# Kernel optimization log

Measured on AMD Instinct MI355X. Metric: run time of the kernel, lower is better.

## Reference

```python
import jax, jax.numpy as jnp
import numpy as np

NUM_EMBEDDINGS = 1024
EMBEDDING_DIM = 256
COMMITMENT_COST = 0.25
DECAY = 0.99
EPS = 1e-5


def setup_inputs() -> dict:
    key = jax.random.key(0)
    k0, k1, k2 = jax.random.split(key, 3)
    x = jax.random.normal(k0, (32, 2048, EMBEDDING_DIM), dtype=jnp.float32)
    # embedding.weight.data.uniform_(-1/K, 1/K)
    embedding_w = jax.random.uniform(
        k1, (NUM_EMBEDDINGS, EMBEDDING_DIM), dtype=jnp.float32,
        minval=-1.0 / NUM_EMBEDDINGS, maxval=1.0 / NUM_EMBEDDINGS)
    ema_cluster_size = jnp.zeros((NUM_EMBEDDINGS,), dtype=jnp.float32)
    ema_w = jax.random.normal(k2, (NUM_EMBEDDINGS, EMBEDDING_DIM), dtype=jnp.float32)
    return {"x": x, "embedding_w": embedding_w,
            "ema_cluster_size": ema_cluster_size, "ema_w": ema_w}


def reference(x, embedding_w, ema_cluster_size, ema_w):
    K, D = embedding_w.shape
    flat = x.reshape(-1, D)  # [N, D]

    # squared L2 distances to codebook: [N, K]
    distances = ((flat * flat).sum(axis=1, keepdims=True)
                 - 2.0 * flat @ embedding_w.T
                 + (embedding_w * embedding_w).sum(axis=1))
    indices = jnp.argmin(distances, axis=1)  # [N] int

    # gather quantized vectors
    quantized = embedding_w[indices].reshape(x.shape)

    # EMA statistics via scatter-add (one-hot.T @ flat without materializing one-hot)
    counts = jax.ops.segment_sum(jnp.ones((flat.shape[0],), dtype=flat.dtype),
                                 indices, num_segments=K)  # [K]
    dw = jax.ops.segment_sum(flat, indices, num_segments=K)  # [K, D]

    new_cluster_size = DECAY * ema_cluster_size + (1.0 - DECAY) * counts
    new_ema_w = DECAY * ema_w + (1.0 - DECAY) * dw

    # Laplace smoothing of cluster sizes, normalized codebook update
    n = new_cluster_size.sum()
    cs = (new_cluster_size + EPS) / (n + K * EPS) * n
    new_embedding_w = new_ema_w / cs[:, None]

    # commitment loss (codebook side is EMA-updated, so only e-latent term)
    e_latent_loss = jnp.mean((jax.lax.stop_gradient(quantized) - x) ** 2)
    loss = COMMITMENT_COST * e_latent_loss

    # straight-through estimator
    quantized_st = x + jax.lax.stop_gradient(quantized - x)

    avg_probs = counts / counts.sum()
    perplexity = jnp.exp(-jnp.sum(avg_probs * jnp.log(avg_probs + 1e-10)))

    return (loss, quantized_st, perplexity,
            new_embedding_w, new_cluster_size, new_ema_w)
```

## Files before the change

### kernel.cpp

```cpp
#include <hip/hip_runtime.h>
#include <math.h>

#define N_ROWS   65536
#define K_EMB    1024
#define D_EMB    256

typedef __attribute__((ext_vector_type(8)))  short short8;
typedef __attribute__((ext_vector_type(4)))  short short4v;
typedef __attribute__((ext_vector_type(16))) float floatx16;

__device__ inline unsigned short f2bf(float f) {
    unsigned u = __float_as_uint(f);
    unsigned r = u + 0x7fffu + ((u >> 16) & 1u);
    return (unsigned short)(r >> 16);
}
__device__ inline float bf2f(unsigned short s) {
    return __uint_as_float(((unsigned)s) << 16);
}

__global__ __launch_bounds__(64)
void prep_e(const float* __restrict__ ew, float* __restrict__ half_esq,
            short* __restrict__ pack_hi, short* __restrict__ pack_lo)
{
    const int k = blockIdx.x;
    const int t = threadIdx.x;
    float4 v = *(const float4*)(ew + (size_t)k * D_EMB + t * 4);
    float s = v.x * v.x + v.y * v.y + v.z * v.z + v.w * v.w;
#pragma unroll
    for (int off = 32; off > 0; off >>= 1) s += __shfl_down(s, off);
    if (t == 0) half_esq[k] = 0.5f * s;

    const int d0   = t * 4;
    const int tile = k >> 5;
    const int kt   = d0 >> 4;
    const int half = (d0 & 15) >> 3;
    const int lane = (k & 31) + 32 * half;
    const int j0   = d0 & 7;
    const int off  = tile * 8192 + kt * 512 + lane * 8 + j0;

    float f[4] = {-v.x, -v.y, -v.z, -v.w};
    short4v h, l;
#pragma unroll
    for (int j = 0; j < 4; ++j) {
        unsigned short hh = f2bf(f[j]);
        h[j] = (short)hh;
        l[j] = (short)f2bf(f[j] - bf2f(hh));
    }
    *(short4v*)(pack_hi + off) = h;
    *(short4v*)(pack_lo + off) = l;
}

__global__ __launch_bounds__(256, 2)
void argmin_mfma(const float* __restrict__ x,
                 const short* __restrict__ pack_hi,
                 const short* __restrict__ pack_lo,
                 const float* __restrict__ half_esq,
                 const float* __restrict__ ew,
                 int* __restrict__ indices,
                 float* __restrict__ out_q,
                 double* __restrict__ loss_buckets)
{
    __shared__ short xs_hi[32 * 256];
    __shared__ short xs_lo[32 * 256];
    __shared__ float cmv[128];
    __shared__ int   cmi[128];
    __shared__ int   widx[32];

    const int t  = threadIdx.x;
    const int r0 = blockIdx.x * 32;

#pragma unroll
    for (int i = 0; i < 4; ++i) {
        int q   = i * 256 + t;
        int row = q >> 5;
        int g8  = q & 31;
        const float* gp = x + (size_t)(r0 + row) * D_EMB + g8 * 8;
        float4 a = *(const float4*)gp;
        float4 b = *(const float4*)(gp + 4);
        float f[8] = {a.x, a.y, a.z, a.w, b.x, b.y, b.z, b.w};
        short8 h8, l8;
#pragma unroll
        for (int j = 0; j < 8; ++j) {
            unsigned short hh = f2bf(f[j]);
            h8[j] = (short)hh;
            l8[j] = (short)f2bf(f[j] - bf2f(hh));
        }
        int off = row * 256 + ((g8 ^ (row & 7)) << 3);
        *(short8*)(xs_hi + off) = h8;
        *(short8*)(xs_lo + off) = l8;
    }
    __syncthreads();

    const int w    = t >> 6;
    const int lane = t & 63;
    const int l31  = lane & 31;
    const int half = lane >> 5;
    const int key  = l31 & 7;
    const short* bbase_h = xs_hi + l31 * 256;
    const short* bbase_l = xs_lo + l31 * 256;

    float mv = 3.4e38f;
    int   mi = 0;

    for (int cp = 0; cp < 4; ++cp) {
        const int c0 = w * 256 + cp * 64;
        const int c1 = c0 + 32;
        const int tile0 = c0 >> 5;

        floatx16 acc0, acc1;
#pragma unroll
        for (int rq = 0; rq < 4; ++rq) {
            float4 e0 = *(const float4*)(half_esq + c0 + rq * 8 + half * 4);
            float4 e1 = *(const float4*)(half_esq + c1 + rq * 8 + half * 4);
            acc0[rq * 4 + 0] = e0.x; acc0[rq * 4 + 1] = e0.y;
            acc0[rq * 4 + 2] = e0.z; acc0[rq * 4 + 3] = e0.w;
            acc1[rq * 4 + 0] = e1.x; acc1[rq * 4 + 1] = e1.y;
            acc1[rq * 4 + 2] = e1.z; acc1[rq * 4 + 3] = e1.w;
        }

        const short* p0h = pack_hi + tile0 * 8192 + lane * 8;
        const short* p0l = pack_lo + tile0 * 8192 + lane * 8;
        const short* p1h = p0h + 8192;
        const short* p1l = p0l + 8192;

        short8 a0h = *(const short8*)(p0h);
        short8 a0l = *(const short8*)(p0l);
        short8 a1h = *(const short8*)(p1h);
        short8 a1l = *(const short8*)(p1l);

#pragma unroll 4
        for (int kt = 0; kt < 16; ++kt) {
            short8 n0h, n0l, n1h, n1l;
            if (kt < 15) {
                n0h = *(const short8*)(p0h + (kt + 1) * 512);
                n0l = *(const short8*)(p0l + (kt + 1) * 512);
                n1h = *(const short8*)(p1h + (kt + 1) * 512);
                n1l = *(const short8*)(p1l + (kt + 1) * 512);
            }
            int coff = (((2 * kt + half) ^ key) << 3);
            short8 bh = *(const short8*)(bbase_h + coff);
            short8 bl = *(const short8*)(bbase_l + coff);
            acc0 = __builtin_amdgcn_mfma_f32_32x32x16_bf16(a0h, bh, acc0, 0, 0, 0);
            acc1 = __builtin_amdgcn_mfma_f32_32x32x16_bf16(a1h, bh, acc1, 0, 0, 0);
            acc0 = __builtin_amdgcn_mfma_f32_32x32x16_bf16(a0h, bl, acc0, 0, 0, 0);
            acc1 = __builtin_amdgcn_mfma_f32_32x32x16_bf16(a1h, bl, acc1, 0, 0, 0);
            acc0 = __builtin_amdgcn_mfma_f32_32x32x16_bf16(a0l, bh, acc0, 0, 0, 0);
            acc1 = __builtin_amdgcn_mfma_f32_32x32x16_bf16(a1l, bh, acc1, 0, 0, 0);
            a0h = n0h; a0l = n0l; a1h = n1h; a1l = n1l;
        }

#pragma unroll
        for (int r = 0; r < 16; ++r) {
            int code0 = c0 + (r & 3) + ((r >> 2) << 3) + half * 4;
            float v0 = acc0[r];
            if (v0 < mv || (v0 == mv && code0 < mi)) { mv = v0; mi = code0; }
            int code1 = code0 + 32;
            float v1 = acc1[r];
            if (v1 < mv || (v1 == mv && code1 < mi)) { mv = v1; mi = code1; }
        }
    }

    {
        float ov = __shfl_xor(mv, 32);
        int   oi = __shfl_xor(mi, 32);
        if (ov < mv || (ov == mv && oi < mi)) { mv = ov; mi = oi; }
    }

    if (half == 0) {
        int slot = w * 32 + l31;
        cmv[slot] = mv;
        cmi[slot] = mi;
    }
    __syncthreads();
    if (t < 32) {
        float bv = cmv[t];
        int   bi = cmi[t];
#pragma unroll
        for (int ww = 1; ww < 4; ++ww) {
            float v = cmv[ww * 32 + t];
            int   i = cmi[ww * 32 + t];
            if (v < bv || (v == bv && i < bi)) { bv = v; bi = i; }
        }
        indices[r0 + t] = bi;
        widx[t] = bi;
    }
    __syncthreads();

    const int g8e  = lane >> 1;
    const int j0e  = (lane & 1) * 4;
    float lsum = 0.0f;
#pragma unroll
    for (int rr = 0; rr < 8; ++rr) {
        const int row = w * 8 + rr;
        const int idx = widx[row];
        const int off = row * 256 + (((g8e) ^ (row & 7)) << 3) + j0e;
        short4v h4 = *(const short4v*)(xs_hi + off);
        short4v l4 = *(const short4v*)(xs_lo + off);
        float xr[4];
#pragma unroll
        for (int j = 0; j < 4; ++j)
            xr[j] = bf2f((unsigned short)h4[j]) + bf2f((unsigned short)l4[j]);
        const float4 ev = *(const float4*)(ew + (size_t)idx * D_EMB + lane * 4);
        float4 q;
        q.x = xr[0] + (ev.x - xr[0]);
        q.y = xr[1] + (ev.y - xr[1]);
        q.z = xr[2] + (ev.z - xr[2]);
        q.w = xr[3] + (ev.w - xr[3]);
        *(float4*)(out_q + (size_t)(r0 + row) * D_EMB + lane * 4) = q;
        float dx = ev.x - xr[0], dy = ev.y - xr[1];
        float dz = ev.z - xr[2], dwv = ev.w - xr[3];
        lsum += dx * dx + dy * dy + dz * dz + dwv * dwv;
    }
#pragma unroll
    for (int off = 32; off > 0; off >>= 1) lsum += __shfl_down(lsum, off);
    if (lane == 0) atomicAdd(&loss_buckets[blockIdx.x & 255], (double)lsum);
}

__global__ __launch_bounds__(256)
void code_stats(const float* __restrict__ x,
                const int* __restrict__ indices,
                float* __restrict__ dw,
                int* __restrict__ counts)
{
    __shared__ int rows[2048];
    __shared__ int nmatch;
    const int k    = blockIdx.x >> 2;
    const int sl   = blockIdx.x & 3;
    const int t    = threadIdx.x;
    const int rbeg = sl * (N_ROWS / 4);
    float sum = 0.0f;
    int total = 0;

    for (int c = 0; c < N_ROWS / 4; c += 2048) {
        if (t == 0) nmatch = 0;
        __syncthreads();
        const int base = rbeg + c + t * 8;
        int4 a = *(const int4*)(indices + base);
        int4 b = *(const int4*)(indices + base + 4);
        int m[8] = {a.x, a.y, a.z, a.w, b.x, b.y, b.z, b.w};
#pragma unroll
        for (int j = 0; j < 8; ++j)
            if (m[j] == k) { int p = atomicAdd(&nmatch, 1); rows[p] = base + j; }
        __syncthreads();
        const int n = nmatch;
        total += n;
        for (int r = 0; r < n; ++r)
            sum += x[(size_t)rows[r] * D_EMB + t];
        __syncthreads();
    }
    if (total > 0) {
        atomicAdd(&dw[(size_t)k * D_EMB + t], sum);
        if (t == 0) atomicAdd(&counts[k], total);
    }
}

__global__ __launch_bounds__(1024)
void finalize_small(const float* __restrict__ ema_cs,
                    const int* __restrict__ counts,
                    const double* __restrict__ loss_buckets,
                    float* __restrict__ cs_ws,
                    float* __restrict__ out_loss,
                    float* __restrict__ out_perp,
                    float* __restrict__ out_ncs)
{
    __shared__ float  red[1024];
    __shared__ double redd[256];
    const int k = threadIdx.x;
    const float cnt = (float)counts[k];
    const float ncs = 0.99f * ema_cs[k] + 0.01f * cnt;
    out_ncs[k] = ncs;
    red[k] = ncs;
    __syncthreads();
    for (int off = 512; off > 0; off >>= 1) {
        if (k < off) red[k] += red[k + off];
        __syncthreads();
    }
    const float n = red[0];
    __syncthreads();
    cs_ws[k] = (ncs + 1e-5f) / (n + 1024.0f * 1e-5f) * n;

    const float p = cnt / 65536.0f;
    red[k] = p * logf(p + 1e-10f);
    if (k < 256) redd[k] = loss_buckets[k];
    __syncthreads();
    for (int off = 512; off > 0; off >>= 1) {
        if (k < off) red[k] += red[k + off];
        __syncthreads();
    }
    if (k == 0) out_perp[0] = expf(-red[0]);
    for (int off = 128; off > 0; off >>= 1) {
        if (k < off) redd[k] += redd[k + off];
        __syncthreads();
    }
    if (k == 0) out_loss[0] = (float)(0.25 * (redd[0] / 16777216.0));
}

__global__ __launch_bounds__(256)
void codebook_kernel(const float* __restrict__ ema_w,
                     const float* __restrict__ dw,
                     const float* __restrict__ cs_ws,
                     float* __restrict__ out_emb,
                     float* __restrict__ out_ema)
{
    const int k = blockIdx.x;
    const int d = threadIdx.x;
    const size_t o = (size_t)k * D_EMB + d;
    const float nev = 0.99f * ema_w[o] + 0.01f * dw[o];
    out_ema[o] = nev;
    out_emb[o] = nev / cs_ws[k];
}

extern "C" void kernel_launch(void* const* d_in, const int* in_sizes, int n_in,
                              void* d_out, int out_size, void* d_ws, size_t ws_size,
                              hipStream_t stream)
{
    const float* x       = (const float*)d_in[0];
    const float* ew      = (const float*)d_in[1];
    const float* ema_cs  = (const float*)d_in[2];
    const float* ema_w   = (const float*)d_in[3];

    float* out       = (float*)d_out;
    float* out_loss  = out;
    float* out_q     = out + 1;
    float* out_perp  = out + 1 + 16777216;
    float* out_emb   = out_perp + 1;
    float* out_ncs   = out_emb + 262144;
    float* out_ema   = out_ncs + 1024;

    char* ws = (char*)d_ws;
    float*  dw           = (float*)(ws);
    int*    counts       = (int*)(ws + 1048576);
    double* loss_buckets = (double*)(ws + 1052672);
    float*  half_esq     = (float*)(ws + 1054720);
    float*  cs_ws        = (float*)(ws + 1058816);
    int*    indices      = (int*)(ws + 1062912);

    short* pack_hi = (short*)(out + 16777220);
    short* pack_lo = (short*)(out + 16777220 + 131072);

    hipMemsetAsync(ws, 0, 1054720, stream);

    prep_e<<<K_EMB, 64, 0, stream>>>(ew, half_esq, pack_hi, pack_lo);
    argmin_mfma<<<N_ROWS / 32, 256, 0, stream>>>(x, pack_hi, pack_lo, half_esq,
                                                 ew, indices, out_q, loss_buckets);
    code_stats<<<K_EMB * 4, 256, 0, stream>>>(x, indices, dw, counts);
    finalize_small<<<1, 1024, 0, stream>>>(ema_cs, counts, loss_buckets, cs_ws,
                                           out_loss, out_perp, out_ncs);
    codebook_kernel<<<K_EMB, 256, 0, stream>>>(ema_w, dw, cs_ws, out_emb, out_ema);
}
```

Measured before the change: 270.0 us.

## Fold workspace zeroing into prep_e, deepen A prefetch, unroll gather sums

Three separate changes. The hipMemsetAsync on the workspace is removed, and the zeroing of dw, counts and the loss buckets moves into the prep_e kernel, which saves one launch/memset on the stream. The MFMA loop now prefetches the codebook fragments two k-steps ahead instead of one and is fully unrolled, to hide more load latency at the cost of extra registers. The code_stats gather loop is unrolled by four, so several independent x loads are in flight at once and the serial add chain is split.

```diff
diff --git a/kernel.cpp b/kernel.cpp
--- a/kernel.cpp
+++ b/kernel.cpp
@@ -20,10 +20,19 @@
 
 __global__ __launch_bounds__(64)
 void prep_e(const float* __restrict__ ew, float* __restrict__ half_esq,
-            short* __restrict__ pack_hi, short* __restrict__ pack_lo)
+            short* __restrict__ pack_hi, short* __restrict__ pack_lo,
+            float* __restrict__ dw, int* __restrict__ counts,
+            double* __restrict__ loss_buckets)
 {
     const int k = blockIdx.x;
     const int t = threadIdx.x;
+
+    *(float4*)(dw + (size_t)k * D_EMB + t * 4) = make_float4(0.f, 0.f, 0.f, 0.f);
+    if (t == 0) {
+        counts[k] = 0;
+        if (k < 256) loss_buckets[k] = 0.0;
+    }
+
     float4 v = *(const float4*)(ew + (size_t)k * D_EMB + t * 4);
     float s = v.x * v.x + v.y * v.y + v.z * v.z + v.w * v.w;
 #pragma unroll
@@ -123,30 +132,35 @@
         const short* p1h = p0h + 8192;
         const short* p1l = p0l + 8192;
 
-        short8 a0h = *(const short8*)(p0h);
-        short8 a0l = *(const short8*)(p0l);
-        short8 a1h = *(const short8*)(p1h);
-        short8 a1l = *(const short8*)(p1l);
-
-#pragma unroll 4
+        short8 c0h = *(const short8*)(p0h);
+        short8 c0l = *(const short8*)(p0l);
+        short8 c1h = *(const short8*)(p1h);
+        short8 c1l = *(const short8*)(p1l);
+        short8 d0h = *(const short8*)(p0h + 512);
+        short8 d0l = *(const short8*)(p0l + 512);
+        short8 d1h = *(const short8*)(p1h + 512);
+        short8 d1l = *(const short8*)(p1l + 512);
+
+#pragma unroll
         for (int kt = 0; kt < 16; ++kt) {
-            short8 n0h, n0l, n1h, n1l;
-            if (kt < 15) {
-                n0h = *(const short8*)(p0h + (kt + 1) * 512);
-                n0l = *(const short8*)(p0l + (kt + 1) * 512);
-                n1h = *(const short8*)(p1h + (kt + 1) * 512);
-                n1l = *(const short8*)(p1l + (kt + 1) * 512);
+            short8 e0h, e0l, e1h, e1l;
+            if (kt < 14) {
+                e0h = *(const short8*)(p0h + (kt + 2) * 512);
+                e0l = *(const short8*)(p0l + (kt + 2) * 512);
+                e1h = *(const short8*)(p1h + (kt + 2) * 512);
+                e1l = *(const short8*)(p1l + (kt + 2) * 512);
             }
             int coff = (((2 * kt + half) ^ key) << 3);
             short8 bh = *(const short8*)(bbase_h + coff);
             short8 bl = *(const short8*)(bbase_l + coff);
-            acc0 = __builtin_amdgcn_mfma_f32_32x32x16_bf16(a0h, bh, acc0, 0, 0, 0);
-            acc1 = __builtin_amdgcn_mfma_f32_32x32x16_bf16(a1h, bh, acc1, 0, 0, 0);
-            acc0 = __builtin_amdgcn_mfma_f32_32x32x16_bf16(a0h, bl, acc0, 0, 0, 0);
-            acc1 = __builtin_amdgcn_mfma_f32_32x32x16_bf16(a1h, bl, acc1, 0, 0, 0);
-            acc0 = __builtin_amdgcn_mfma_f32_32x32x16_bf16(a0l, bh, acc0, 0, 0, 0);
-            acc1 = __builtin_amdgcn_mfma_f32_32x32x16_bf16(a1l, bh, acc1, 0, 0, 0);
-            a0h = n0h; a0l = n0l; a1h = n1h; a1l = n1l;
+            acc0 = __builtin_amdgcn_mfma_f32_32x32x16_bf16(c0h, bh, acc0, 0, 0, 0);
+            acc1 = __builtin_amdgcn_mfma_f32_32x32x16_bf16(c1h, bh, acc1, 0, 0, 0);
+            acc0 = __builtin_amdgcn_mfma_f32_32x32x16_bf16(c0h, bl, acc0, 0, 0, 0);
+            acc1 = __builtin_amdgcn_mfma_f32_32x32x16_bf16(c1h, bl, acc1, 0, 0, 0);
+            acc0 = __builtin_amdgcn_mfma_f32_32x32x16_bf16(c0l, bh, acc0, 0, 0, 0);
+            acc1 = __builtin_amdgcn_mfma_f32_32x32x16_bf16(c1l, bh, acc1, 0, 0, 0);
+            c0h = d0h; c0l = d0l; c1h = d1h; c1l = d1l;
+            d0h = e0h; d0l = e0l; d1h = e1h; d1l = e1l;
         }
 
 #pragma unroll
@@ -244,7 +258,16 @@
         __syncthreads();
         const int n = nmatch;
         total += n;
-        for (int r = 0; r < n; ++r)
+        int r = 0;
+        for (; r + 4 <= n; r += 4) {
+            int i0 = rows[r], i1 = rows[r + 1], i2 = rows[r + 2], i3 = rows[r + 3];
+            float v0 = x[(size_t)i0 * D_EMB + t];
+            float v1 = x[(size_t)i1 * D_EMB + t];
+            float v2 = x[(size_t)i2 * D_EMB + t];
+            float v3 = x[(size_t)i3 * D_EMB + t];
+            sum += (v0 + v1) + (v2 + v3);
+        }
+        for (; r < n; ++r)
             sum += x[(size_t)rows[r] * D_EMB + t];
         __syncthreads();
     }
@@ -338,9 +361,8 @@
     short* pack_hi = (short*)(out + 16777220);
     short* pack_lo = (short*)(out + 16777220 + 131072);
 
-    hipMemsetAsync(ws, 0, 1054720, stream);
-
-    prep_e<<<K_EMB, 64, 0, stream>>>(ew, half_esq, pack_hi, pack_lo);
+    prep_e<<<K_EMB, 64, 0, stream>>>(ew, half_esq, pack_hi, pack_lo,
+                                     dw, counts, loss_buckets);
     argmin_mfma<<<N_ROWS / 32, 256, 0, stream>>>(x, pack_hi, pack_lo, half_esq,
                                                  ew, indices, out_q, loss_buckets);
     code_stats<<<K_EMB * 4, 256, 0, stream>>>(x, indices, dw, counts);
```

New measurement: 324.2 us. 20.1% more time.
